# Kernel optimization log

Hardware: AMD Instinct MI355X
Metric: run time of the kernel (lower is better)

## Reference

```python
import jax, jax.numpy as jnp
import numpy as np

N_NODES = 50000
N_EDGES = 800000
DIM = 96
N_LAYERS = 3
N_GRAPHS = 128
OUT_DIM = 10


def setup_inputs() -> dict:
    key = jax.random.key(0)
    ks = jax.random.split(key, 9)
    s = 1.0 / np.sqrt(DIM)
    return {
        "x": jax.random.normal(ks[0], (N_NODES, DIM), dtype=jnp.float32),
        "edge_index": jax.random.randint(ks[1], (2, N_EDGES), 0, N_NODES, dtype=jnp.int32),
        "batch": jnp.sort(jax.random.randint(ks[2], (N_NODES,), 0, N_GRAPHS, dtype=jnp.int32)),
        "W1": jax.random.normal(ks[3], (N_LAYERS, DIM, DIM), dtype=jnp.float32) * s,
        "W2": jax.random.normal(ks[4], (N_LAYERS, DIM, DIM), dtype=jnp.float32) * s,
        "cw1": jax.random.normal(ks[5], (DIM, DIM), dtype=jnp.float32) * s,
        "cb1": jax.random.normal(ks[6], (DIM,), dtype=jnp.float32) * s,
        "cw2": jax.random.normal(ks[7], (DIM, OUT_DIM), dtype=jnp.float32) * s,
        "cb2": jax.random.normal(ks[8], (OUT_DIM,), dtype=jnp.float32) * s,
    }


def reference(x, edge_index, batch, W1, W2, cw1, cb1, cw2, cb2):
    src, dst = edge_index[0], edge_index[1]
    h = x
    for l in range(N_LAYERS):
        self_part = h @ W1[l]                       # [N, D]
        # transform at node level then gather per edge (same math as per-edge W2(x_j))
        msg = (h @ W2[l])[src]                      # [E, D]
        neighbor_part = jax.ops.segment_sum(msg, dst, num_segments=N_NODES)
        h = jax.nn.relu(self_part + neighbor_part)
    graph_emb = jax.ops.segment_sum(h, batch, num_segments=N_GRAPHS)  # [G, D]
    hidden = jax.nn.relu(graph_emb @ cw1 + cb1)
    return hidden @ cw2 + cb2                       # [G, OUT_DIM]
```

## Files before the change

kernel.cpp:

```cpp
#include <hip/hip_runtime.h>

#define N_NODES   50000
#define N_EDGES   800000
#define DIM       96
#define N_GRAPHS  128
#define OUT_DIM   10
#define NPAD      50048
#define NBINS     391
#define P1_BLOCKS 128
#define EPB       (N_EDGES / P1_BLOCKS)
#define SLICECAP  48
#define CAP       64
#define LPAD      104

#define CAST_NB   ((N_NODES * 12 + 255) / 256)
#define CONV_NB   ((3 * DIM * 2 * DIM + 255) / 256)

typedef __attribute__((ext_vector_type(8))) short          short8;
typedef __attribute__((ext_vector_type(8))) unsigned short u16x8;
typedef __attribute__((ext_vector_type(4))) float          f32x4;

__device__ __forceinline__ float b2f(unsigned short u) {
    union { unsigned int i; float f; } v; v.i = ((unsigned int)u) << 16; return v.f;
}
__device__ __forceinline__ unsigned short f2b(float f) {
    union { float f; unsigned int i; } v; v.f = f;
    unsigned int u = v.i;
    return (unsigned short)((u + 0x7fffu + ((u >> 16) & 1u)) >> 16);
}

__global__ __launch_bounds__(256) void prep_pass1(
    const float* __restrict__ x,  const float* __restrict__ W1,
    const float* __restrict__ W2, const int* __restrict__ src,
    const int* __restrict__ dst,  unsigned short* __restrict__ harr,
    unsigned short* __restrict__ Bt, int* __restrict__ binned,
    int* __restrict__ cnt)
{
    __shared__ int cur[NBINS];
    const int b = blockIdx.x;
    const int t = threadIdx.x;

    if (b < P1_BLOCKS) {
        const int e0 = b * EPB;
        for (int i = t; i < NBINS; i += 256) cur[i] = 0;
        __syncthreads();
        for (int e = e0 + t; e < e0 + EPB; e += 256) {
            const int d   = dst[e];
            const int bin = d >> 7;
            const int pos = atomicAdd(&cur[bin], 1);
            if (pos < SLICECAP)
                binned[((size_t)bin * P1_BLOCKS + b) * SLICECAP + pos]
                    = ((d & 127) << 16) | src[e];
        }
        __syncthreads();
        for (int i = t; i < NBINS; i += 256)
            cnt[i * P1_BLOCKS + b] = min(cur[i], SLICECAP);
    } else if (b < P1_BLOCKS + CAST_NB) {
        const int tid = (b - P1_BLOCKS) * 256 + t;
        if (tid >= N_NODES * 12) return;
        const int node = tid / 12;
        const int c    = (tid - node * 12) * 8;
        const float4 v0 = *(const float4*)(x + (size_t)node * DIM + c);
        const float4 v1 = *(const float4*)(x + (size_t)node * DIM + c + 4);
        u16x8 o;
        o[0] = f2b(v0.x); o[1] = f2b(v0.y); o[2] = f2b(v0.z); o[3] = f2b(v0.w);
        o[4] = f2b(v1.x); o[5] = f2b(v1.y); o[6] = f2b(v1.z); o[7] = f2b(v1.w);
        *(u16x8*)(harr + (size_t)node * DIM + c) = o;
    } else {
        const int idx = (b - P1_BLOCKS - CAST_NB) * 256 + t;
        if (idx >= 3 * DIM * 2 * DIM) return;
        const int l   = idx / (DIM * 2 * DIM);
        const int rem = idx - l * (DIM * 2 * DIM);
        const int n   = rem / (2 * DIM);
        const int k   = rem - n * (2 * DIM);
        const float v = (k < DIM) ? W1[(size_t)l * DIM * DIM + k * DIM + n]
                                  : W2[(size_t)l * DIM * DIM + (k - DIM) * DIM + n];
        Bt[idx] = f2b(v);
    }
}

__global__ __launch_bounds__(256) void pass2_scatter(const int* __restrict__ cnt,
                                                     const int* __restrict__ binned,
                                                     int* __restrict__ csrc,
                                                     int* __restrict__ deg)
{
    __shared__ int ncnt[128];
    const int bin = blockIdx.x;
    const int t   = threadIdx.x;
    const int n0  = bin << 7;

    if (t < 128) ncnt[t] = 0;
    __syncthreads();

    const int slice = t >> 1;
    const int par   = t & 1;
    const int c     = cnt[bin * P1_BLOCKS + slice];
    const int* __restrict__ bb = binned + ((size_t)bin * P1_BLOCKS + slice) * SLICECAP;

    for (int i = par; i < c; i += 2) {
        const int v    = bb[i];
        const int dlow = v >> 16;
        const int s    = v & 0xffff;
        const int pos  = atomicAdd(&ncnt[dlow], 1);
        if (pos < CAP) csrc[(size_t)(n0 + dlow) * CAP + pos] = s;
    }
    __syncthreads();

    if (t < 128 && n0 + t < N_NODES) deg[n0 + t] = min(ncnt[t], CAP);
}

__global__ __launch_bounds__(384) void gnn_layer(
    const unsigned short* __restrict__ harr, const int* __restrict__ deg,
    const int* __restrict__ csrc, const unsigned short* __restrict__ Btl,
    unsigned short* __restrict__ hout)
{
    __shared__ unsigned short aggLds[64][LPAD];
    const int t       = threadIdx.x;
    const int rowBase = blockIdx.x * 64;

    const int lane = t & 63;
    const int w    = t >> 6;
    const int m    = lane & 15;
    const int q    = lane >> 4;
    short8 bfrag[6];
#pragma unroll
    for (int s = 0; s < 6; s++)
        bfrag[s] = *(const short8*)(Btl + (size_t)(w * 16 + m) * (2 * DIM) + s * 32 + q * 8);

    {
        const int r    = t / 6;
        const int sub  = t - r * 6;
        const int node = rowBase + r;
        const int off  = sub * 16;

        float a[16];
#pragma unroll
        for (int i = 0; i < 16; i++) a[i] = 0.f;

        if (node < N_NODES) {
            const int d = deg[node];
            const int* __restrict__ bkt = csrc + (size_t)node * CAP;
            const unsigned short* __restrict__ hb = harr + off;

            const int nfull = d & ~3;
            int c = 0;
            for (; c < nfull; c += 4) {
                const int4 s = *(const int4*)(bkt + c);
                const unsigned short* p0 = hb + (size_t)s.x * DIM;
                const unsigned short* p1 = hb + (size_t)s.y * DIM;
                const unsigned short* p2 = hb + (size_t)s.z * DIM;
                const unsigned short* p3 = hb + (size_t)s.w * DIM;
                const u16x8 va0 = *(const u16x8*)(p0), vb0 = *(const u16x8*)(p0 + 8);
                const u16x8 va1 = *(const u16x8*)(p1), vb1 = *(const u16x8*)(p1 + 8);
                const u16x8 va2 = *(const u16x8*)(p2), vb2 = *(const u16x8*)(p2 + 8);
                const u16x8 va3 = *(const u16x8*)(p3), vb3 = *(const u16x8*)(p3 + 8);
#pragma unroll
                for (int i = 0; i < 8; i++) {
                    a[i]     += b2f(va0[i]) + b2f(va1[i]) + b2f(va2[i]) + b2f(va3[i]);
                    a[i + 8] += b2f(vb0[i]) + b2f(vb1[i]) + b2f(vb2[i]) + b2f(vb3[i]);
                }
            }
            for (; c < d; c++) {
                const unsigned short* p0 = hb + (size_t)bkt[c] * DIM;
                const u16x8 va0 = *(const u16x8*)(p0), vb0 = *(const u16x8*)(p0 + 8);
#pragma unroll
                for (int i = 0; i < 8; i++) {
                    a[i]     += b2f(va0[i]);
                    a[i + 8] += b2f(vb0[i]);
                }
            }
        }

        u16x8 o0, o1;
#pragma unroll
        for (int i = 0; i < 8; i++) { o0[i] = f2b(a[i]); o1[i] = f2b(a[i + 8]); }
        *(u16x8*)(&aggLds[r][off])     = o0;
        *(u16x8*)(&aggLds[r][off + 8]) = o1;
    }
    __syncthreads();

    f32x4 accv[4];
#pragma unroll
    for (int r = 0; r < 4; r++) {
        const int rb = rowBase + r * 16;
        f32x4 acc = {0.f, 0.f, 0.f, 0.f};
        const unsigned short* ah = harr + (size_t)(rb + m) * DIM + q * 8;
#pragma unroll
        for (int s = 0; s < 3; s++) {
            const short8 af = *(const short8*)(ah + s * 32);
            acc = __builtin_amdgcn_mfma_f32_16x16x32_bf16(af, bfrag[s], acc, 0, 0, 0);
        }
#pragma unroll
        for (int s = 0; s < 3; s++) {
            const short8 af = *(const short8*)(&aggLds[r * 16 + m][s * 32 + q * 8]);
            acc = __builtin_amdgcn_mfma_f32_16x16x32_bf16(af, bfrag[s + 3], acc, 0, 0, 0);
        }
        accv[r] = acc;
    }
    __syncthreads();

#pragma unroll
    for (int r = 0; r < 4; r++)
#pragma unroll
        for (int i = 0; i < 4; i++)
            aggLds[r * 16 + q * 4 + i][w * 16 + m] = f2b(fmaxf(accv[r][i], 0.f));
    __syncthreads();

#pragma unroll
    for (int k = 0; k < 2; k++) {
        const int idx = t + k * 384;
        const int row = idx / 12;
        const int ch  = idx - row * 12;
        const int grow = rowBase + row;
        if (grow < N_NODES)
            *(u16x8*)(hout + (size_t)grow * DIM + ch * 8)
                = *(const u16x8*)(&aggLds[row][ch * 8]);
    }
}

__global__ __launch_bounds__(960) void pool_classify(
    const unsigned short* __restrict__ h, const int* __restrict__ batch,
    const float* __restrict__ cw1, const float* __restrict__ cb1,
    const float* __restrict__ cw2, const float* __restrict__ cb2,
    float* __restrict__ out)
{
    const int g = blockIdx.x;
    const int t = threadIdx.x;

    int lo = 0, hi = N_NODES;
    while (lo < hi) { int m = (lo + hi) >> 1; if (batch[m] < g) lo = m + 1; else hi = m; }
    const int start = lo;
    hi = N_NODES;
    while (lo < hi) { int m = (lo + hi) >> 1; if (batch[m] < g + 1) lo = m + 1; else hi = m; }
    const int end = lo;

    __shared__ float part[10][DIM];
    __shared__ float gr[DIM];
    __shared__ float hid[DIM];

    const int col = t % DIM;
    const int ty  = t / DIM;

    float s = 0.f;
    for (int n = start + ty; n < end; n += 10)
        s += b2f(h[(size_t)n * DIM + col]);
    part[ty][col] = s;
    __syncthreads();
    if (ty == 0) {
        float acc = 0.f;
#pragma unroll
        for (int p = 0; p < 10; p++) acc += part[p][col];
        gr[col] = acc;
    }
    __syncthreads();

    if (ty < 4) {
        float hsum = 0.f;
        const int k0 = ty * (DIM / 4);
#pragma unroll 4
        for (int k = k0; k < k0 + DIM / 4; k++)
            hsum += gr[k] * cw1[k * DIM + col];
        part[ty][col] = hsum;
    }
    __syncthreads();
    if (ty == 0)
        hid[col] = fmaxf(part[0][col] + part[1][col] + part[2][col] + part[3][col]
                         + cb1[col], 0.f);
    __syncthreads();

    if (t < OUT_DIM) {
        float o = cb2[t];
#pragma unroll 4
        for (int k = 0; k < DIM; k++) o += hid[k] * cw2[k * OUT_DIM + t];
        out[g * OUT_DIM + t] = o;
    }
}

extern "C" void kernel_launch(void* const* d_in, const int* in_sizes, int n_in,
                              void* d_out, int out_size, void* d_ws, size_t ws_size,
                              hipStream_t stream)
{
    const float* x     = (const float*)d_in[0];
    const int*   ei    = (const int*)  d_in[1];
    const int*   batch = (const int*)  d_in[2];
    const float* W1    = (const float*)d_in[3];
    const float* W2    = (const float*)d_in[4];
    const float* cw1   = (const float*)d_in[5];
    const float* cb1   = (const float*)d_in[6];
    const float* cw2   = (const float*)d_in[7];
    const float* cb2   = (const float*)d_in[8];
    float*       out   = (float*)d_out;

    const int* src = ei;
    const int* dst = ei + N_EDGES;

    unsigned short* bufA = (unsigned short*)d_ws;
    unsigned short* bufB = bufA + (size_t)NPAD * DIM;
    unsigned short* Bt   = bufB + (size_t)NPAD * DIM;
    int*   cnt    = (int*)(Bt + 3 * DIM * 2 * DIM);
    int*   binned = cnt + NBINS * P1_BLOCKS;
    int*   csrc   = binned + (size_t)NBINS * P1_BLOCKS * SLICECAP;
    int*   deg    = csrc + (size_t)N_NODES * CAP;

    prep_pass1<<<P1_BLOCKS + CAST_NB + CONV_NB, 256, 0, stream>>>(
        x, W1, W2, src, dst, bufA, Bt, binned, cnt);
    pass2_scatter<<<NBINS, 256, 0, stream>>>(cnt, binned, csrc, deg);

    unsigned short* hin  = bufA;
    unsigned short* hout = bufB;
    for (int l = 0; l < 3; l++) {
        gnn_layer<<<NPAD / 64, 384, 0, stream>>>(hin, deg, csrc,
                                                 Bt + (size_t)l * DIM * 2 * DIM, hout);
        unsigned short* tmp = hin; hin = hout; hout = tmp;
    }

    pool_classify<<<N_GRAPHS, 960, 0, stream>>>(hin, batch, cw1, cb1, cw2, cb2, out);
}
```

Measured before the change: 253.9 us.

## Halve rows per block in gnn_layer and split gather across 12 threads per node

Each gnn_layer block now handles 32 nodes instead of 64, so twice as many blocks launch. Each node's neighbor gather is split across 12 threads, each loading 8 features instead of 16, and the edge loop is unrolled by 8. The goal is more memory-level parallelism and better load balance in the latency-bound gather. In exchange, the B fragments are reloaded by twice as many blocks and each block does less MFMA work.

```diff
diff --git a/kernel.cpp b/kernel.cpp
--- a/kernel.cpp
+++ b/kernel.cpp
@@ -114,9 +114,9 @@
     const int* __restrict__ csrc, const unsigned short* __restrict__ Btl,
     unsigned short* __restrict__ hout)
 {
-    __shared__ unsigned short aggLds[64][LPAD];
+    __shared__ unsigned short aggLds[32][LPAD];
     const int t       = threadIdx.x;
-    const int rowBase = blockIdx.x * 64;
+    const int rowBase = blockIdx.x * 32;
 
     const int lane = t & 63;
     const int w    = t >> 6;
@@ -128,60 +128,65 @@
         bfrag[s] = *(const short8*)(Btl + (size_t)(w * 16 + m) * (2 * DIM) + s * 32 + q * 8);
 
     {
-        const int r    = t / 6;
-        const int sub  = t - r * 6;
+        const int r    = t / 12;
+        const int sub  = t - r * 12;
         const int node = rowBase + r;
-        const int off  = sub * 16;
-
-        float a[16];
-#pragma unroll
-        for (int i = 0; i < 16; i++) a[i] = 0.f;
+        const int off  = sub * 8;
+
+        float a[8];
+#pragma unroll
+        for (int i = 0; i < 8; i++) a[i] = 0.f;
 
         if (node < N_NODES) {
             const int d = deg[node];
             const int* __restrict__ bkt = csrc + (size_t)node * CAP;
             const unsigned short* __restrict__ hb = harr + off;
 
-            const int nfull = d & ~3;
             int c = 0;
-            for (; c < nfull; c += 4) {
+            for (; c + 8 <= d; c += 8) {
+                const int4 s0 = *(const int4*)(bkt + c);
+                const int4 s1 = *(const int4*)(bkt + c + 4);
+                const u16x8 v0 = *(const u16x8*)(hb + (size_t)s0.x * DIM);
+                const u16x8 v1 = *(const u16x8*)(hb + (size_t)s0.y * DIM);
+                const u16x8 v2 = *(const u16x8*)(hb + (size_t)s0.z * DIM);
+                const u16x8 v3 = *(const u16x8*)(hb + (size_t)s0.w * DIM);
+                const u16x8 v4 = *(const u16x8*)(hb + (size_t)s1.x * DIM);
+                const u16x8 v5 = *(const u16x8*)(hb + (size_t)s1.y * DIM);
+                const u16x8 v6 = *(const u16x8*)(hb + (size_t)s1.z * DIM);
+                const u16x8 v7 = *(const u16x8*)(hb + (size_t)s1.w * DIM);
+#pragma unroll
+                for (int i = 0; i < 8; i++)
+                    a[i] += b2f(v0[i]) + b2f(v1[i]) + b2f(v2[i]) + b2f(v3[i])
+                          + b2f(v4[i]) + b2f(v5[i]) + b2f(v6[i]) + b2f(v7[i]);
+            }
+            if (c + 4 <= d) {
                 const int4 s = *(const int4*)(bkt + c);
-                const unsigned short* p0 = hb + (size_t)s.x * DIM;
-                const unsigned short* p1 = hb + (size_t)s.y * DIM;
-                const unsigned short* p2 = hb + (size_t)s.z * DIM;
-                const unsigned short* p3 = hb + (size_t)s.w * DIM;
-                const u16x8 va0 = *(const u16x8*)(p0), vb0 = *(const u16x8*)(p0 + 8);
-                const u16x8 va1 = *(const u16x8*)(p1), vb1 = *(const u16x8*)(p1 + 8);
-                const u16x8 va2 = *(const u16x8*)(p2), vb2 = *(const u16x8*)(p2 + 8);
-                const u16x8 va3 = *(const u16x8*)(p3), vb3 = *(const u16x8*)(p3 + 8);
-#pragma unroll
-                for (int i = 0; i < 8; i++) {
-                    a[i]     += b2f(va0[i]) + b2f(va1[i]) + b2f(va2[i]) + b2f(va3[i]);
-                    a[i + 8] += b2f(vb0[i]) + b2f(vb1[i]) + b2f(vb2[i]) + b2f(vb3[i]);
-                }
+                const u16x8 v0 = *(const u16x8*)(hb + (size_t)s.x * DIM);
+                const u16x8 v1 = *(const u16x8*)(hb + (size_t)s.y * DIM);
+                const u16x8 v2 = *(const u16x8*)(hb + (size_t)s.z * DIM);
+                const u16x8 v3 = *(const u16x8*)(hb + (size_t)s.w * DIM);
+#pragma unroll
+                for (int i = 0; i < 8; i++)
+                    a[i] += b2f(v0[i]) + b2f(v1[i]) + b2f(v2[i]) + b2f(v3[i]);
+                c += 4;
             }
             for (; c < d; c++) {
-                const unsigned short* p0 = hb + (size_t)bkt[c] * DIM;
-                const u16x8 va0 = *(const u16x8*)(p0), vb0 = *(const u16x8*)(p0 + 8);
-#pragma unroll
-                for (int i = 0; i < 8; i++) {
-                    a[i]     += b2f(va0[i]);
-                    a[i + 8] += b2f(vb0[i]);
-                }
+                const u16x8 v0 = *(const u16x8*)(hb + (size_t)bkt[c] * DIM);
+#pragma unroll
+                for (int i = 0; i < 8; i++) a[i] += b2f(v0[i]);
             }
         }
 
-        u16x8 o0, o1;
-#pragma unroll
-        for (int i = 0; i < 8; i++) { o0[i] = f2b(a[i]); o1[i] = f2b(a[i + 8]); }
-        *(u16x8*)(&aggLds[r][off])     = o0;
-        *(u16x8*)(&aggLds[r][off + 8]) = o1;
-    }
-    __syncthreads();
-
-    f32x4 accv[4];
-#pragma unroll
-    for (int r = 0; r < 4; r++) {
+        u16x8 o;
+#pragma unroll
+        for (int i = 0; i < 8; i++) o[i] = f2b(a[i]);
+        *(u16x8*)(&aggLds[r][off]) = o;
+    }
+    __syncthreads();
+
+    f32x4 accv[2];
+#pragma unroll
+    for (int r = 0; r < 2; r++) {
         const int rb = rowBase + r * 16;
         f32x4 acc = {0.f, 0.f, 0.f, 0.f};
         const unsigned short* ah = harr + (size_t)(rb + m) * DIM + q * 8;
@@ -200,17 +205,15 @@
     __syncthreads();
 
 #pragma unroll
-    for (int r = 0; r < 4; r++)
+    for (int r = 0; r < 2; r++)
 #pragma unroll
         for (int i = 0; i < 4; i++)
             aggLds[r * 16 + q * 4 + i][w * 16 + m] = f2b(fmaxf(accv[r][i], 0.f));
     __syncthreads();
 
-#pragma unroll
-    for (int k = 0; k < 2; k++) {
-        const int idx = t + k * 384;
-        const int row = idx / 12;
-        const int ch  = idx - row * 12;
+    {
+        const int row = t / 12;
+        const int ch  = t - row * 12;
         const int grow = rowBase + row;
         if (grow < N_NODES)
             *(u16x8*)(hout + (size_t)grow * DIM + ch * 8)
@@ -309,7 +312,7 @@
     unsigned short* hin  = bufA;
     unsigned short* hout = bufB;
     for (int l = 0; l < 3; l++) {
-        gnn_layer<<<NPAD / 64, 384, 0, stream>>>(hin, deg, csrc,
+        gnn_layer<<<NPAD / 32, 384, 0, stream>>>(hin, deg, csrc,
                                                  Bt + (size_t)l * DIM * 2 * DIM, hout);
         unsigned short* tmp = hin; hin = hout; hout = tmp;
     }
```

Measured after the change: 256.2 us. Within noise of the previous version (+0.9%).
